# Kernel optimization log

Hardware: AMD Instinct MI355X
Metric: run time of the kernel (lower is better)

Reference implementation:

```python
import jax, jax.numpy as jnp
import numpy as np

ALPHA = 0.2  # LeakyReLU negative slope


def gat_layer(x, W, a, alpha=ALPHA):
    """Multi-head dense GAT layer.
    x: (B, N, F); W: (H, F, O); a: (H, 2*O, 1).
    Returns (B, N, H*O) — ELU(head outputs) concatenated over heads.
    """
    H, F, O = W.shape
    Wh = jnp.einsum('bnf,hfo->bhno', x, W)          # (B,H,N,O)
    a_src = a[:, :O, 0]                              # (H,O)
    a_dst = a[:, O:, 0]                              # (H,O)
    s_src = jnp.einsum('bhno,ho->bhn', Wh, a_src)    # (B,H,N)
    s_dst = jnp.einsum('bhno,ho->bhn', Wh, a_dst)    # (B,H,N)
    e = s_src[..., :, None] + s_dst[..., None, :]    # (B,H,N,N)
    e = jax.nn.leaky_relu(e, negative_slope=alpha)
    att = jax.nn.softmax(e, axis=-1)                 # softmax over neighbors j
    out = jnp.einsum('bhnm,bhmo->bhno', att, Wh)     # (B,H,N,O)
    out = jax.nn.elu(out)
    B, _, N, _ = out.shape
    return jnp.transpose(out, (0, 2, 1, 3)).reshape(B, N, H * O)


def setup_inputs() -> dict:
    key = jax.random.key(0)
    ks = jax.random.split(key, 5)
    B, N = 32, 1024
    x = jax.random.normal(ks[0], (B, N, 4), dtype=jnp.float32)
    # layer1: nfeat=4, nhid=2, nheads=3
    W1 = jax.random.normal(ks[1], (3, 4, 2), dtype=jnp.float32) * 0.5
    a1 = jax.random.normal(ks[2], (3, 4, 1), dtype=jnp.float32) * 0.5
    # layer2: nfeat=6, nhid=4, nheads=1
    W2 = jax.random.normal(ks[3], (1, 6, 4), dtype=jnp.float32) * 0.5
    a2 = jax.random.normal(ks[4], (1, 8, 1), dtype=jnp.float32) * 0.5
    return {"x": x, "W1": W1, "a1": a1, "W2": W2, "a2": a2}


def reference(x, W1, a1, W2, a2):
    h = gat_layer(x, W1, a1)   # (B, N, 6)
    y = gat_layer(h, W2, a2)   # (B, N, 4)
    return y
```

## Files before the change

### kernel.cpp

```cpp
#include <hip/hip_runtime.h>


#define GAT_ALPHA 0.2f
#define LOG2E 1.44269504088896f

template <int F, int O, int H, int RPB>
__global__ __launch_bounds__(256) void gat_layer_kernel(
    const float* __restrict__ x,
    const float* __restrict__ Wt,
    const float* __restrict__ at,
    float* __restrict__ out)
{
    constexpr int N = 1024, NT = 256, S = 16;
    constexpr int R = RPB / 16;
    constexpr int Q = O + 1;
    constexpr int CHUNKS = N / RPB;
    constexpr int PAD = R * Q + 1;

    const int bid   = blockIdx.x;
    const int chunk = bid % CHUNKS;
    const int h     = (bid / CHUNKS) % H;
    const int b     = bid / (CHUNKS * H);
    const int tid   = threadIdx.x;
    const int wv    = tid >> 6;
    const int l     = tid & 63;
    const int r     = (l >> 2) & 15;
    const int sq    = l & 3;
    const int s     = (wv << 2) | sq;

    float Wl[F][4];
#pragma unroll
    for (int f = 0; f < F; ++f)
#pragma unroll
        for (int o = 0; o < O; ++o) Wl[f][o] = Wt[(h * F + f) * O + o];
    float asrc[4], adst[4];
#pragma unroll
    for (int o = 0; o < O; ++o) {
        asrc[o] = at[h * 2 * O + o];
        adst[o] = at[h * 2 * O + O + o];
    }

    __shared__ float4 sEW[N];
    __shared__ float2 sW2[(O > 2) ? N : 1];
    __shared__ float  sred[4];
    __shared__ float  sredu[4 * 16 * PAD];

    const float* xb = x + (size_t)b * N * F;
    float dmax = -3.0e38f;
    for (int m = tid; m < N; m += NT) {
        float xv[F];
        if constexpr (F == 4) {
            const float4 v = ((const float4*)xb)[m];
            xv[0] = v.x; xv[1] = v.y; xv[2] = v.z; xv[3] = v.w;
        } else {
#pragma unroll
            for (int k = 0; k < F / 2; ++k) {
                const float2 v = ((const float2*)xb)[m * (F / 2) + k];
                xv[2 * k] = v.x; xv[2 * k + 1] = v.y;
            }
        }
        float wh[4], d = 0.0f;
#pragma unroll
        for (int o = 0; o < O; ++o) {
            float acc = 0.0f;
#pragma unroll
            for (int f = 0; f < F; ++f) acc += xv[f] * Wl[f][o];
            wh[o] = acc; d += acc * adst[o];
        }
        sEW[m] = make_float4(d, 0.0f, wh[0], wh[1]);
        if constexpr (O > 2) sW2[m] = make_float2(wh[2], wh[3]);
        dmax = fmaxf(dmax, d);
    }
#pragma unroll
    for (int off = 32; off; off >>= 1) dmax = fmaxf(dmax, __shfl_xor(dmax, off, 64));
    if (l == 0) sred[wv] = dmax;
    __syncthreads();
    const float D = fmaxf(fmaxf(sred[0], sred[1]), fmaxf(sred[2], sred[3]));

    float c1[R], c2[R];
#pragma unroll
    for (int j = 0; j < R; ++j) {
        const int row = chunk * RPB + r + 16 * j;
        const float4 ew = sEW[row];
        float sn = ew.z * asrc[0] + ew.w * asrc[1];
        if constexpr (O > 2) {
            const float2 w2 = sW2[row];
            sn += w2.x * asrc[2] + w2.y * asrc[3];
        }
        const float z = sn + D;
        const float e = __builtin_amdgcn_exp2f(-0.8f * LOG2E * fabsf(z));
        c1[j] = (z >= 0.0f) ? 1.0f : e;
        c2[j] = (z >= 0.0f) ? e : 1.0f;
    }

    for (int m = tid; m < N; m += NT) {
        const float t = (sEW[m].x - D) * LOG2E;
        sEW[m].x = __builtin_amdgcn_exp2f(t);
        sEW[m].y = __builtin_amdgcn_exp2f(GAT_ALPHA * t);
    }
    __syncthreads();

    float den[R], num[R][4];
#pragma unroll
    for (int j = 0; j < R; ++j) {
        den[j] = 0.0f;
#pragma unroll
        for (int o = 0; o < 4; ++o) num[j][o] = 0.0f;
    }

#pragma unroll 4
    for (int mi = 0; mi < N / S; ++mi) {
        const int m = mi * S + s;
        const float4 ew = sEW[m];
        float w2x = 0.0f, w2y = 0.0f;
        if constexpr (O > 2) { const float2 t2 = sW2[m]; w2x = t2.x; w2y = t2.y; }
#pragma unroll
        for (int j = 0; j < R; ++j) {
            const float wgt = fmaxf(c1[j] * ew.x, c2[j] * ew.y);
            den[j]    += wgt;
            num[j][0] += wgt * ew.z;
            num[j][1] += wgt * ew.w;
            if constexpr (O > 2) {
                num[j][2] += wgt * w2x;
                num[j][3] += wgt * w2y;
            }
        }
    }

#pragma unroll
    for (int j = 0; j < R; ++j) {
        den[j] += __shfl_xor(den[j], 1, 64);
        den[j] += __shfl_xor(den[j], 2, 64);
#pragma unroll
        for (int o = 0; o < O; ++o) {
            num[j][o] += __shfl_xor(num[j][o], 1, 64);
            num[j][o] += __shfl_xor(num[j][o], 2, 64);
        }
    }
    if (sq == 0) {
#pragma unroll
        for (int j = 0; j < R; ++j) {
            const int base = (wv * 16 + r) * PAD + j * Q;
            sredu[base] = den[j];
#pragma unroll
            for (int o = 0; o < O; ++o) sredu[base + 1 + o] = num[j][o];
        }
    }
    __syncthreads();

    for (int idx = tid; idx < RPB * O; idx += NT) {
        const int rowl = idx / O, o = idx % O;
        const int rr = rowl & 15, jj = rowl >> 4;
        float dn = 0.0f, nm = 0.0f;
#pragma unroll
        for (int ww = 0; ww < 4; ++ww) {
            const int base = (ww * 16 + rr) * PAD + jj * Q;
            dn += sredu[base];
            nm += sredu[base + 1 + o];
        }
        float v = nm / dn;
        v = (v > 0.0f) ? v : (__expf(v) - 1.0f);
        const int row = chunk * RPB + rowl;
        out[((size_t)b * N + row) * (H * O) + h * O + o] = v;
    }
}

extern "C" void kernel_launch(void* const* d_in, const int* in_sizes, int n_in,
                              void* d_out, int out_size, void* d_ws, size_t ws_size,
                              hipStream_t stream) {
    const float* x  = (const float*)d_in[0];
    const float* W1 = (const float*)d_in[1];
    const float* a1 = (const float*)d_in[2];
    const float* W2 = (const float*)d_in[3];
    const float* a2 = (const float*)d_in[4];

    float* h1 = (float*)d_ws;
    float* y  = (float*)d_out;

    constexpr int B = 32;
    gat_layer_kernel<4, 2, 3, 64><<<B * 3 * 16, 256, 0, stream>>>(x, W1, a1, h1);
    gat_layer_kernel<6, 4, 1, 64><<<B * 1 * 16, 256, 0, stream>>>(h1, W2, a2, y);
}
```

Measured before the change: 94.66 us.

## Pair neighbor columns into packed float2 math and enlarge layer-1 row chunks

```diff
diff --git a/kernel.cpp b/kernel.cpp
--- a/kernel.cpp
+++ b/kernel.cpp
@@ -3,6 +3,8 @@
 
 #define GAT_ALPHA 0.2f
 #define LOG2E 1.44269504088896f
+
+typedef float v2f __attribute__((ext_vector_type(2)));
 
 template <int F, int O, int H, int RPB>
 __global__ __launch_bounds__(256) void gat_layer_kernel(
@@ -12,6 +14,7 @@
     float* __restrict__ out)
 {
     constexpr int N = 1024, NT = 256, S = 16;
+    constexpr int NP = N / 2;
     constexpr int R = RPB / 16;
     constexpr int Q = O + 1;
     constexpr int CHUNKS = N / RPB;
@@ -28,48 +31,65 @@
     const int sq    = l & 3;
     const int s     = (wv << 2) | sq;
 
-    float Wl[F][4];
+    float Wl[F][O];
 #pragma unroll
     for (int f = 0; f < F; ++f)
 #pragma unroll
         for (int o = 0; o < O; ++o) Wl[f][o] = Wt[(h * F + f) * O + o];
-    float asrc[4], adst[4];
+    float asrc[O], adst[O];
 #pragma unroll
     for (int o = 0; o < O; ++o) {
         asrc[o] = at[h * 2 * O + o];
         adst[o] = at[h * 2 * O + O + o];
     }
 
-    __shared__ float4 sEW[N];
-    __shared__ float2 sW2[(O > 2) ? N : 1];
+    __shared__ float2 sd2[NP];
+    __shared__ float4 sE[NP];
+    __shared__ float4 sW01[NP];
+    __shared__ float4 sW23[(O > 2) ? NP : 1];
     __shared__ float  sred[4];
     __shared__ float  sredu[4 * 16 * PAD];
 
     const float* xb = x + (size_t)b * N * F;
     float dmax = -3.0e38f;
-    for (int m = tid; m < N; m += NT) {
-        float xv[F];
+#pragma unroll
+    for (int qq = 0; qq < NP / NT; ++qq) {
+        const int q = qq * NT + tid;
+        float xv[2][F];
         if constexpr (F == 4) {
-            const float4 v = ((const float4*)xb)[m];
-            xv[0] = v.x; xv[1] = v.y; xv[2] = v.z; xv[3] = v.w;
+            const float4 va = ((const float4*)xb)[2 * q];
+            const float4 vb = ((const float4*)xb)[2 * q + 1];
+            xv[0][0] = va.x; xv[0][1] = va.y; xv[0][2] = va.z; xv[0][3] = va.w;
+            xv[1][0] = vb.x; xv[1][1] = vb.y; xv[1][2] = vb.z; xv[1][3] = vb.w;
         } else {
-#pragma unroll
-            for (int k = 0; k < F / 2; ++k) {
-                const float2 v = ((const float2*)xb)[m * (F / 2) + k];
-                xv[2 * k] = v.x; xv[2 * k + 1] = v.y;
+            const float4* x4 = (const float4*)xb;
+            const float2* x2 = (const float2*)xb;
+            const float4 fa = x4[3 * q];
+            const float2 fb = x2[6 * q + 2];
+            const float2 fc = x2[6 * q + 3];
+            const float4 fd = x4[3 * q + 2];
+            xv[0][0] = fa.x; xv[0][1] = fa.y; xv[0][2] = fa.z; xv[0][3] = fa.w;
+            xv[0][4] = fb.x; xv[0][5] = fb.y;
+            xv[1][0] = fc.x; xv[1][1] = fc.y;
+            xv[1][2] = fd.x; xv[1][3] = fd.y; xv[1][4] = fd.z; xv[1][5] = fd.w;
+        }
+        float wh[2][O], d[2];
+#pragma unroll
+        for (int p = 0; p < 2; ++p) {
+            d[p] = 0.0f;
+#pragma unroll
+            for (int o = 0; o < O; ++o) {
+                float acc = 0.0f;
+#pragma unroll
+                for (int f = 0; f < F; ++f) acc += xv[p][f] * Wl[f][o];
+                wh[p][o] = acc; d[p] += acc * adst[o];
             }
         }
-        float wh[4], d = 0.0f;
-#pragma unroll
-        for (int o = 0; o < O; ++o) {
-            float acc = 0.0f;
-#pragma unroll
-            for (int f = 0; f < F; ++f) acc += xv[f] * Wl[f][o];
-            wh[o] = acc; d += acc * adst[o];
-        }
-        sEW[m] = make_float4(d, 0.0f, wh[0], wh[1]);
-        if constexpr (O > 2) sW2[m] = make_float2(wh[2], wh[3]);
-        dmax = fmaxf(dmax, d);
+        sd2[q]  = make_float2(d[0], d[1]);
+        sW01[q] = make_float4(wh[0][0], wh[1][0], wh[0][1], wh[1][1]);
+        if constexpr (O > 2)
+            sW23[q] = make_float4(wh[0][2], wh[1][2], wh[0][3], wh[1][3]);
+        dmax = fmaxf(dmax, fmaxf(d[0], d[1]));
     }
 #pragma unroll
     for (int off = 32; off; off >>= 1) dmax = fmaxf(dmax, __shfl_xor(dmax, off, 64));
@@ -77,73 +97,90 @@
     __syncthreads();
     const float D = fmaxf(fmaxf(sred[0], sred[1]), fmaxf(sred[2], sred[3]));
 
+#pragma unroll
+    for (int qq = 0; qq < NP / NT; ++qq) {
+        const int q = qq * NT + tid;
+        const float2 dp = sd2[q];
+        const float t0 = (dp.x - D) * LOG2E;
+        const float t1 = (dp.y - D) * LOG2E;
+        sE[q] = make_float4(__builtin_amdgcn_exp2f(t0),
+                            __builtin_amdgcn_exp2f(t1),
+                            __builtin_amdgcn_exp2f(GAT_ALPHA * t0),
+                            __builtin_amdgcn_exp2f(GAT_ALPHA * t1));
+    }
+
     float c1[R], c2[R];
 #pragma unroll
     for (int j = 0; j < R; ++j) {
         const int row = chunk * RPB + r + 16 * j;
-        const float4 ew = sEW[row];
-        float sn = ew.z * asrc[0] + ew.w * asrc[1];
+        const int qr = row >> 1, cp = row & 1;
+        const float4 w01 = sW01[qr];
+        float sn = (cp ? w01.y : w01.x) * asrc[0] + (cp ? w01.w : w01.z) * asrc[1];
         if constexpr (O > 2) {
-            const float2 w2 = sW2[row];
-            sn += w2.x * asrc[2] + w2.y * asrc[3];
+            const float4 w23 = sW23[qr];
+            sn += (cp ? w23.y : w23.x) * asrc[2] + (cp ? w23.w : w23.z) * asrc[3];
         }
         const float z = sn + D;
         const float e = __builtin_amdgcn_exp2f(-0.8f * LOG2E * fabsf(z));
         c1[j] = (z >= 0.0f) ? 1.0f : e;
         c2[j] = (z >= 0.0f) ? e : 1.0f;
     }
-
-    for (int m = tid; m < N; m += NT) {
-        const float t = (sEW[m].x - D) * LOG2E;
-        sEW[m].x = __builtin_amdgcn_exp2f(t);
-        sEW[m].y = __builtin_amdgcn_exp2f(GAT_ALPHA * t);
-    }
     __syncthreads();
 
-    float den[R], num[R][4];
+    v2f den[R], num[R][O];
 #pragma unroll
     for (int j = 0; j < R; ++j) {
-        den[j] = 0.0f;
-#pragma unroll
-        for (int o = 0; o < 4; ++o) num[j][o] = 0.0f;
+        den[j] = (v2f)(0.0f);
+#pragma unroll
+        for (int o = 0; o < O; ++o) num[j][o] = (v2f)(0.0f);
     }
 
 #pragma unroll 4
-    for (int mi = 0; mi < N / S; ++mi) {
-        const int m = mi * S + s;
-        const float4 ew = sEW[m];
-        float w2x = 0.0f, w2y = 0.0f;
-        if constexpr (O > 2) { const float2 t2 = sW2[m]; w2x = t2.x; w2y = t2.y; }
+    for (int p = 0; p < NP / S; ++p) {
+        const int q = p * S + s;
+        const float4 e4 = sE[q];
+        const float4 w4 = sW01[q];
+        const v2f E1 = {e4.x, e4.y}, E2 = {e4.z, e4.w};
+        const v2f W0 = {w4.x, w4.y}, W1 = {w4.z, w4.w};
+        v2f W2, W3;
+        if constexpr (O > 2) {
+            const float4 w4b = sW23[q];
+            W2 = (v2f){w4b.x, w4b.y}; W3 = (v2f){w4b.z, w4b.w};
+        }
 #pragma unroll
         for (int j = 0; j < R; ++j) {
-            const float wgt = fmaxf(c1[j] * ew.x, c2[j] * ew.y);
-            den[j]    += wgt;
-            num[j][0] += wgt * ew.z;
-            num[j][1] += wgt * ew.w;
+            const v2f A = c1[j] * E1;
+            const v2f Bv = c2[j] * E2;
+            v2f w;
+            w.x = fmaxf(A.x, Bv.x);
+            w.y = fmaxf(A.y, Bv.y);
+            den[j] += w;
+            num[j][0] += w * W0;
+            num[j][1] += w * W1;
             if constexpr (O > 2) {
-                num[j][2] += wgt * w2x;
-                num[j][3] += wgt * w2y;
+                num[j][2] += w * W2;
+                num[j][3] += w * W3;
             }
         }
     }
 
 #pragma unroll
     for (int j = 0; j < R; ++j) {
-        den[j] += __shfl_xor(den[j], 1, 64);
-        den[j] += __shfl_xor(den[j], 2, 64);
+        float dn = den[j].x + den[j].y;
+        dn += __shfl_xor(dn, 1, 64);
+        dn += __shfl_xor(dn, 2, 64);
+        float nm[O];
 #pragma unroll
         for (int o = 0; o < O; ++o) {
-            num[j][o] += __shfl_xor(num[j][o], 1, 64);
-            num[j][o] += __shfl_xor(num[j][o], 2, 64);
-        }
-    }
-    if (sq == 0) {
-#pragma unroll
-        for (int j = 0; j < R; ++j) {
+            nm[o] = num[j][o].x + num[j][o].y;
+            nm[o] += __shfl_xor(nm[o], 1, 64);
+            nm[o] += __shfl_xor(nm[o], 2, 64);
+        }
+        if (sq == 0) {
             const int base = (wv * 16 + r) * PAD + j * Q;
-            sredu[base] = den[j];
-#pragma unroll
-            for (int o = 0; o < O; ++o) sredu[base + 1 + o] = num[j][o];
+            sredu[base] = dn;
+#pragma unroll
+            for (int o = 0; o < O; ++o) sredu[base + 1 + o] = nm[o];
         }
     }
     __syncthreads();
@@ -178,6 +215,6 @@
     float* y  = (float*)d_out;
 
     constexpr int B = 32;
-    gat_layer_kernel<4, 2, 3, 64><<<B * 3 * 16, 256, 0, stream>>>(x, W1, a1, h1);
+    gat_layer_kernel<4, 2, 3, 128><<<B * 3 * 8, 256, 0, stream>>>(x, W1, a1, h1);
     gat_layer_kernel<6, 4, 1, 64><<<B * 1 * 16, 256, 0, stream>>>(h1, W2, a2, y);
 }
```

Result: faster. 85.73 us (-9.4%).
